# Performance work log

Measured on AMD Instinct MI355X. Metric: run time of the kernel, lower is better.

## Reference

```python
import jax, jax.numpy as jnp
import numpy as np

B, S, D = 4, 4096, 2048
NUM_MODALITIES = 2


def setup_inputs() -> dict:
    key = jax.random.key(0)
    k_x, k_t, k_w0, k_b0, k_w1, k_b1 = jax.random.split(key, 6)
    scale = 1.0 / np.sqrt(D)
    return {
        "hidden_states": jax.random.normal(k_x, (B, S, D), dtype=jnp.float32),
        "type_ids": jax.random.randint(k_t, (B, S), 0, NUM_MODALITIES, dtype=jnp.int32),
        "W0": jax.random.uniform(k_w0, (D, D), jnp.float32, -scale, scale),
        "b0": jax.random.uniform(k_b0, (D,), jnp.float32, -scale, scale),
        "W1": jax.random.uniform(k_w1, (D, D), jnp.float32, -scale, scale),
        "b1": jax.random.uniform(k_b1, (D,), jnp.float32, -scale, scale),
    }


def reference(hidden_states, type_ids, W0, b0, W1, b1):
    # Original: gather tokens where type_ids == i, apply expert i's Linear,
    # scatter into a zero-init [B, S, out_dim] buffer. The masks partition
    # all tokens, so this equals a masked mixture of the two dense GEMMs.
    y0 = jnp.einsum("bsd,ed->bse", hidden_states, W0) + b0  # expert 0
    y1 = jnp.einsum("bsd,ed->bse", hidden_states, W1) + b1  # expert 1
    m0 = (type_ids == 0)[..., None]
    m1 = (type_ids == 1)[..., None]
    zero = jnp.zeros((), dtype=y0.dtype)
    return jnp.where(m0, y0, zero) + jnp.where(m1, y1, zero)
```

## Files before the change

### kernel.cpp

```cpp
#include <hip/hip_runtime.h>
#include <hip/hip_bf16.h>
#include <stdint.h>


#define T_TOK 16384
#define DDIM  2048
#define NT_K  32
#define NT_D  64
#define MT    64
#define NTILE 8

typedef __attribute__((ext_vector_type(4))) float          f32x4;
typedef __attribute__((ext_vector_type(8))) short          bf16x8;
typedef __attribute__((ext_vector_type(2))) unsigned int   u32x2;

#define WS_HBF   0ull
#define WS_W0BF  67108864ull
#define WS_W1BF  75497472ull
#define WS_META  83886080ull
#define WS_IDX   83886208ull
#define WS_NEED  (WS_IDX + 65536ull)

__device__ __forceinline__ unsigned short cvt1_bf16(float f) {
  unsigned u = __builtin_bit_cast(unsigned, f);
  unsigned rnd = 0x7fffu + ((u >> 16) & 1u);
  return (unsigned short)((u + rnd) >> 16);
}

__device__ __forceinline__ void gload_lds16(const void* g, void* l) {
  __builtin_amdgcn_global_load_lds(
      (const __attribute__((address_space(1))) unsigned int*)g,
      (__attribute__((address_space(3))) unsigned int*)l, 16, 0, 0);
}

#define BAR()     asm volatile("s_barrier" ::: "memory")
#define VMCNT2()  asm volatile("s_waitcnt vmcnt(2)" ::: "memory")
#define VMCNT4()  asm volatile("s_waitcnt vmcnt(4)" ::: "memory")
#define VMCNT6()  asm volatile("s_waitcnt vmcnt(6)" ::: "memory")
#define VMCNT0()  asm volatile("s_waitcnt vmcnt(0)" ::: "memory")
#define LGKM0()   asm volatile("s_waitcnt lgkmcnt(0)" ::: "memory")
#define SCHEDBAR() __builtin_amdgcn_sched_barrier(0)

__global__ void k_prep(const float* __restrict__ H, const float* __restrict__ W0,
                       const float* __restrict__ W1, const int* __restrict__ typ,
                       unsigned short* __restrict__ Hbf,
                       unsigned short* __restrict__ W0bf,
                       unsigned short* __restrict__ W1bf,
                       int* __restrict__ meta, int* __restrict__ idx) {
  const int gid = blockIdx.x * blockDim.x + threadIdx.x;
  if (gid < T_TOK) {
    int t = typ[gid];
    int pos = (t == 0) ? atomicAdd(&meta[0], 1)
                       : (T_TOK - 1) - atomicAdd(&meta[1], 1);
    idx[pos] = gid;
  }
  const int nH = T_TOK * DDIM / 4;
  const int nW = DDIM * DDIM / 4;
  const int total = nH + 2 * nW;
  const int stride = gridDim.x * blockDim.x;
  for (int i = gid; i < total; i += stride) {
    const float* s; unsigned short* d; int j;
    if (i < nH)           { s = H;  d = Hbf;  j = i; }
    else if (i < nH + nW) { s = W0; d = W0bf; j = i - nH; }
    else                  { s = W1; d = W1bf; j = i - nH - nW; }
    f32x4 v = ((const f32x4*)s)[j];
    unsigned p0 = (unsigned)cvt1_bf16(v[0]) | ((unsigned)cvt1_bf16(v[1]) << 16);
    unsigned p1 = (unsigned)cvt1_bf16(v[2]) | ((unsigned)cvt1_bf16(v[3]) << 16);
    u32x2 o; o[0] = p0; o[1] = p1;
    ((u32x2*)d)[j] = o;
  }
}

__global__ __launch_bounds__(512) void k_gemm256(
    const unsigned short* __restrict__ Hbf,
    const unsigned short* __restrict__ W0bf,
    const unsigned short* __restrict__ W1bf,
    const float* __restrict__ B0, const float* __restrict__ B1,
    const int* __restrict__ meta, const int* __restrict__ idx,
    float* __restrict__ OUT)
{
  __shared__ char lds[147456];

  const int orig = blockIdx.x;
  const int wg = (orig & 7) * 64 + (orig >> 3);
  int my = wg >> 3;
  const int bx = wg & 7;

  const int c0 = meta[0];
  int ms = c0 >> 8; if (ms > MT - 1) ms = MT - 1;
  my = (my == 0) ? ms : (my == ms) ? 0 : my;

  const int tid  = threadIdx.x;
  const int lane = tid & 63;
  const int wid  = tid >> 6;
  const int wr   = wid >> 2;
  const int wc   = wid & 3;
  const int fr   = lane & 15;
  const int g    = lane >> 4;

  const int start = my * 256;
  const int isDual = (start < c0 && c0 < start + 256) ? 1 : 0;
  const int e0    = (start >= c0) ? 1 : 0;
  const int colBase = bx * 256;

  const int cs = (lane & 3) ^ ((lane >> 3) & 3);
  const char* aS[2];
  int rt[2];
#pragma unroll
  for (int l = 0; l < 2; ++l) {
    int ch = 2 * wid + l;
    rt[l] = ch * 16 + (lane >> 2);
    int orow = idx[start + rt[l]];
    aS[l] = (const char*)Hbf + (size_t)orow * 4096 + cs * 16;
  }
  const int chB = (2 * wid) * 1024;

  const int sw = (g ^ ((fr >> 1) & 3)) << 4;
  int aF[8], bF[4];
#pragma unroll
  for (int m = 0; m < 8; ++m) aF[m] = ((wr * 128 + m * 16 + fr) << 6) + sw;
#pragma unroll
  for (int n = 0; n < 4; ++n) bF[n] = ((wc * 64 + n * 16 + fr) << 6) + sw;

  f32x4 acc[8][4];
#pragma unroll
  for (int m = 0; m < 8; ++m)
#pragma unroll
    for (int n = 0; n < 4; ++n) acc[m][n] = (f32x4)0.0f;

  int cols[4];
#pragma unroll
  for (int n = 0; n < 4; ++n) cols[n] = colBase + wc * 64 + n * 16 + fr;

  if (!isDual) {
    const unsigned short* Wb = e0 ? W1bf : W0bf;
    const char* wS[2];
#pragma unroll
    for (int l = 0; l < 2; ++l)
      wS[l] = (const char*)(Wb + (size_t)(colBase + rt[l]) * DDIM) + cs * 16;

    auto STAGE_A = [&](int d, int kh, int tn) {
      char* dst = lds + (d << 15) + (kh << 14) + chB;
      int ko = tn * 128 + kh * 64;
      gload_lds16(aS[0] + ko, dst);
      gload_lds16(aS[1] + ko, dst + 1024);
    };
    auto STAGE_B = [&](int d, int kh, int tn) {
      char* dst = lds + 65536 + (d << 15) + (kh << 14) + chB;
      int ko = tn * 128 + kh * 64;
      gload_lds16(wS[0] + ko, dst);
      gload_lds16(wS[1] + ko, dst + 1024);
    };

    STAGE_A(0, 0, 0); STAGE_B(0, 0, 0); STAGE_A(0, 1, 0); STAGE_B(0, 1, 0);
    VMCNT4();
    BAR();

#pragma unroll 2
    for (int t = 0; t < NT_K; ++t) {
      const int c = t & 1, d = c ^ 1;
      int t1 = t + 1; if (t1 == NT_K) t1 = NT_K - 1;
      const char* Ak0 = lds + (c << 15);
      const char* Ak1 = Ak0 + 16384;
      const char* Bk0 = lds + 65536 + (c << 15);
      const char* Bk1 = Bk0 + 16384;

      bf16x8 a[8], bb0, bb1;

#pragma unroll
      for (int m = 0; m < 8; ++m) a[m] = *(const bf16x8*)(Ak0 + aF[m]);
      bb0 = *(const bf16x8*)(Bk0 + bF[0]);
      bb1 = *(const bf16x8*)(Bk0 + bF[1]);
      STAGE_A(d, 0, t1);
      BAR(); LGKM0(); SCHEDBAR();
      __builtin_amdgcn_s_setprio(1);
#pragma unroll
      for (int m = 0; m < 8; ++m) {
        acc[m][0] = __builtin_amdgcn_mfma_f32_16x16x32_bf16(a[m], bb0, acc[m][0], 0, 0, 0);
        acc[m][1] = __builtin_amdgcn_mfma_f32_16x16x32_bf16(a[m], bb1, acc[m][1], 0, 0, 0);
      }
      __builtin_amdgcn_s_setprio(0);

      bb0 = *(const bf16x8*)(Bk0 + bF[2]);
      bb1 = *(const bf16x8*)(Bk0 + bF[3]);
      VMCNT2();
      STAGE_B(d, 0, t1);
      BAR(); LGKM0(); SCHEDBAR();
      __builtin_amdgcn_s_setprio(1);
#pragma unroll
      for (int m = 0; m < 8; ++m) {
        acc[m][2] = __builtin_amdgcn_mfma_f32_16x16x32_bf16(a[m], bb0, acc[m][2], 0, 0, 0);
        acc[m][3] = __builtin_amdgcn_mfma_f32_16x16x32_bf16(a[m], bb1, acc[m][3], 0, 0, 0);
      }
      __builtin_amdgcn_s_setprio(0);

#pragma unroll
      for (int m = 0; m < 8; ++m) a[m] = *(const bf16x8*)(Ak1 + aF[m]);
      bb0 = *(const bf16x8*)(Bk1 + bF[0]);
      bb1 = *(const bf16x8*)(Bk1 + bF[1]);
      STAGE_A(d, 1, t1);
      BAR(); LGKM0(); SCHEDBAR();
      __builtin_amdgcn_s_setprio(1);
#pragma unroll
      for (int m = 0; m < 8; ++m) {
        acc[m][0] = __builtin_amdgcn_mfma_f32_16x16x32_bf16(a[m], bb0, acc[m][0], 0, 0, 0);
        acc[m][1] = __builtin_amdgcn_mfma_f32_16x16x32_bf16(a[m], bb1, acc[m][1], 0, 0, 0);
      }
      __builtin_amdgcn_s_setprio(0);

      bb0 = *(const bf16x8*)(Bk1 + bF[2]);
      bb1 = *(const bf16x8*)(Bk1 + bF[3]);
      VMCNT2();
      STAGE_B(d, 1, t1);
      BAR(); LGKM0(); SCHEDBAR();
      __builtin_amdgcn_s_setprio(1);
#pragma unroll
      for (int m = 0; m < 8; ++m) {
        acc[m][2] = __builtin_amdgcn_mfma_f32_16x16x32_bf16(a[m], bb0, acc[m][2], 0, 0, 0);
        acc[m][3] = __builtin_amdgcn_mfma_f32_16x16x32_bf16(a[m], bb1, acc[m][3], 0, 0, 0);
      }
      __builtin_amdgcn_s_setprio(0);
    }

    VMCNT0();

    const float* Bv = e0 ? B1 : B0;
    float bias[4];
#pragma unroll
    for (int n = 0; n < 4; ++n) bias[n] = Bv[cols[n]];
#pragma unroll
    for (int m = 0; m < 8; ++m) {
      int lb = wr * 128 + m * 16 + (g << 2);
#pragma unroll
      for (int j = 0; j < 4; ++j) {
        int orow = idx[start + lb + j];
        float* op = OUT + (size_t)orow * DDIM;
#pragma unroll
        for (int n = 0; n < 4; ++n) op[cols[n]] = acc[m][n][j] + bias[n];
      }
    }
  } else {
    const char* wS0[2]; const char* wS1[2];
#pragma unroll
    for (int l = 0; l < 2; ++l) {
      wS0[l] = (const char*)(W0bf + (size_t)(colBase + rt[l]) * DDIM) + cs * 16;
      wS1[l] = (const char*)(W1bf + (size_t)(colBase + rt[l]) * DDIM) + cs * 16;
    }
    const int lo_w = c0 - start - wr * 128;
    int mmix = 8;
    if (lo_w > 0 && lo_w < 128 && (lo_w & 15)) mmix = lo_w >> 4;

    f32x4 accX[4];
#pragma unroll
    for (int n = 0; n < 4; ++n) accX[n] = (f32x4)0.0f;

    auto DSTAGE = [&](int d, int tn) {
      int ko = tn * 64;
      char* ad  = lds + d * 16384 + chB;
      char* b0d = lds + 49152 + d * 16384 + chB;
      char* b1d = lds + 98304 + d * 16384 + chB;
      gload_lds16(aS[0] + ko, ad);
      gload_lds16(aS[1] + ko, ad + 1024);
      gload_lds16(wS0[0] + ko, b0d);
      gload_lds16(wS0[1] + ko, b0d + 1024);
      gload_lds16(wS1[0] + ko, b1d);
      gload_lds16(wS1[1] + ko, b1d + 1024);
    };

    DSTAGE(0, 0); DSTAGE(1, 1);
    VMCNT6();
    BAR();

    for (int t = 0; t < NT_D; ++t) {
      const int c = t % 3;
      const int d = (t + 2) % 3;
      int t2 = t + 2; if (t2 >= NT_D) t2 = NT_D - 1;
      const char* Ac  = lds + c * 16384;
      const char* B0c = lds + 49152 + c * 16384;
      const char* B1c = lds + 98304 + c * 16384;
      bf16x8 a[8], b0f[4], b1f[4];
#pragma unroll
      for (int m = 0; m < 8; ++m) a[m] = *(const bf16x8*)(Ac + aF[m]);
#pragma unroll
      for (int n = 0; n < 4; ++n) {
        b0f[n] = *(const bf16x8*)(B0c + bF[n]);
        b1f[n] = *(const bf16x8*)(B1c + bF[n]);
      }
      DSTAGE(d, t2);
      VMCNT6();
      BAR(); LGKM0(); SCHEDBAR();
      __builtin_amdgcn_s_setprio(1);
#pragma unroll
      for (int m = 0; m < 8; ++m) {
        if (m == mmix) {
#pragma unroll
          for (int n = 0; n < 4; ++n) {
            acc[m][n] = __builtin_amdgcn_mfma_f32_16x16x32_bf16(a[m], b0f[n], acc[m][n], 0, 0, 0);
            accX[n]   = __builtin_amdgcn_mfma_f32_16x16x32_bf16(a[m], b1f[n], accX[n],   0, 0, 0);
          }
        } else if (m * 16 >= lo_w) {
#pragma unroll
          for (int n = 0; n < 4; ++n)
            acc[m][n] = __builtin_amdgcn_mfma_f32_16x16x32_bf16(a[m], b1f[n], acc[m][n], 0, 0, 0);
        } else {
#pragma unroll
          for (int n = 0; n < 4; ++n)
            acc[m][n] = __builtin_amdgcn_mfma_f32_16x16x32_bf16(a[m], b0f[n], acc[m][n], 0, 0, 0);
        }
      }
      __builtin_amdgcn_s_setprio(0);
      BAR();
    }
    VMCNT0();

    float bias0v[4], bias1v[4];
#pragma unroll
    for (int n = 0; n < 4; ++n) { bias0v[n] = B0[cols[n]]; bias1v[n] = B1[cols[n]]; }
#pragma unroll
    for (int m = 0; m < 8; ++m) {
      int lb = wr * 128 + m * 16 + (g << 2);
      if (m == mmix) {
#pragma unroll
        for (int j = 0; j < 4; ++j) {
          int p = start + lb + j;
          int orow = idx[p];
          float* op = OUT + (size_t)orow * DDIM;
          if (p >= c0) {
#pragma unroll
            for (int n = 0; n < 4; ++n) op[cols[n]] = accX[n][j] + bias1v[n];
          } else {
#pragma unroll
            for (int n = 0; n < 4; ++n) op[cols[n]] = acc[m][n][j] + bias0v[n];
          }
        }
      } else {
        int em = (m * 16 >= lo_w) ? 1 : 0;
#pragma unroll
        for (int j = 0; j < 4; ++j) {
          int orow = idx[start + lb + j];
          float* op = OUT + (size_t)orow * DDIM;
#pragma unroll
          for (int n = 0; n < 4; ++n)
            op[cols[n]] = acc[m][n][j] + (em ? bias1v[n] : bias0v[n]);
        }
      }
    }
  }
}

#define BMd 64
#define BNd 64
#define BKd 32
#define LDW 36

__device__ __forceinline__ bf16x8 cvt_bf16x8(f32x4 lo, f32x4 hi) {
  bf16x8 r;
#pragma unroll
  for (int i = 0; i < 4; ++i) {
    r[i]     = (short)cvt1_bf16(lo[i]);
    r[i + 4] = (short)cvt1_bf16(hi[i]);
  }
  return r;
}

__global__ __launch_bounds__(256, 2) void mot_mfma_diag(
    const float* __restrict__ H,  const int* __restrict__ TYP,
    const float* __restrict__ W0, const float* __restrict__ B0,
    const float* __restrict__ W1, const float* __restrict__ B1,
    float* __restrict__ OUT)
{
  __shared__ float As[BMd * LDW];
  __shared__ float W0s[BNd * LDW];
  __shared__ float W1s[BNd * LDW];

  const int tid = threadIdx.x;
  const int rowBase = blockIdx.y * BMd;
  const int colBase = blockIdx.x * BNd;
  const int srow  = tid >> 3;
  const int scol4 = (tid & 7) << 2;
  const float* hA  = H  + (size_t)(rowBase + srow) * DDIM + scol4;
  const float* hW0 = W0 + (size_t)(colBase + srow) * DDIM + scol4;
  const float* hW1 = W1 + (size_t)(colBase + srow) * DDIM + scol4;

  const int lane = tid & 63;
  const int w    = tid >> 6;
  const int fr   = lane & 15;
  const int g    = lane >> 4;

  f32x4 acc0[4], acc1[4];
#pragma unroll
  for (int m = 0; m < 4; ++m) { acc0[m] = (f32x4)0.0f; acc1[m] = (f32x4)0.0f; }

  for (int k0 = 0; k0 < DDIM; k0 += BKd) {
    f32x4 va[2], v0[2], v1[2];
#pragma unroll
    for (int p = 0; p < 2; ++p) {
      va[p] = *(const f32x4*)(hA  + (size_t)p * 32 * DDIM);
      v0[p] = *(const f32x4*)(hW0 + (size_t)p * 32 * DDIM);
      v1[p] = *(const f32x4*)(hW1 + (size_t)p * 32 * DDIM);
    }
    hA += BKd; hW0 += BKd; hW1 += BKd;
    __syncthreads();
#pragma unroll
    for (int p = 0; p < 2; ++p) {
      int r = srow + 32 * p;
      *(f32x4*)(&As [r * LDW + scol4]) = va[p];
      *(f32x4*)(&W0s[r * LDW + scol4]) = v0[p];
      *(f32x4*)(&W1s[r * LDW + scol4]) = v1[p];
    }
    __syncthreads();

    bf16x8 af[4];
#pragma unroll
    for (int m = 0; m < 4; ++m) {
      const float* ap = &As[(m * 16 + fr) * LDW + g * 8];
      af[m] = cvt_bf16x8(*(const f32x4*)ap, *(const f32x4*)(ap + 4));
    }
    const float* b0p = &W0s[(w * 16 + fr) * LDW + g * 8];
    const float* b1p = &W1s[(w * 16 + fr) * LDW + g * 8];
    bf16x8 bf0 = cvt_bf16x8(*(const f32x4*)b0p, *(const f32x4*)(b0p + 4));
    bf16x8 bf1 = cvt_bf16x8(*(const f32x4*)b1p, *(const f32x4*)(b1p + 4));
#pragma unroll
    for (int m = 0; m < 4; ++m) {
      acc0[m] = __builtin_amdgcn_mfma_f32_16x16x32_bf16(af[m], bf0, acc0[m], 0, 0, 0);
      acc1[m] = __builtin_amdgcn_mfma_f32_16x16x32_bf16(af[m], bf1, acc1[m], 0, 0, 0);
    }
  }

  const int col = colBase + w * 16 + fr;
  const float bz0 = B0[col];
  const float bz1 = B1[col];
#pragma unroll
  for (int m = 0; m < 4; ++m)
#pragma unroll
    for (int j = 0; j < 4; ++j) {
      int row = rowBase + m * 16 + (g << 2) + j;
      int t = TYP[row];
      OUT[(size_t)row * DDIM + col] = (t == 0) ? (acc0[m][j] + bz0) : (acc1[m][j] + bz1);
    }
}

extern "C" void kernel_launch(void* const* d_in, const int* in_sizes, int n_in,
                              void* d_out, int out_size, void* d_ws, size_t ws_size,
                              hipStream_t stream) {
  const float* H   = (const float*)d_in[0];
  const int*   TYP = (const int*)  d_in[1];
  const float* W0  = (const float*)d_in[2];
  const float* B0v = (const float*)d_in[3];
  const float* W1  = (const float*)d_in[4];
  const float* B1v = (const float*)d_in[5];
  float* OUT = (float*)d_out;

  if (ws_size < WS_NEED) {
    dim3 grid(DDIM / BNd, T_TOK / BMd);
    mot_mfma_diag<<<grid, dim3(256), 0, stream>>>(H, TYP, W0, B0v, W1, B1v, OUT);
    return;
  }

  unsigned short* Hbf  = (unsigned short*)((char*)d_ws + WS_HBF);
  unsigned short* W0bf = (unsigned short*)((char*)d_ws + WS_W0BF);
  unsigned short* W1bf = (unsigned short*)((char*)d_ws + WS_W1BF);
  int* meta = (int*)((char*)d_ws + WS_META);
  int* idx  = (int*)((char*)d_ws + WS_IDX);

  hipMemsetAsync(meta, 0, 16, stream);
  k_prep<<<4096, 256, 0, stream>>>(H, W0, W1, TYP, Hbf, W0bf, W1bf, meta, idx);
  k_gemm256<<<MT * NTILE, 512, 0, stream>>>(Hbf, W0bf, W1bf, B0v, B1v, meta, idx, OUT);
}
```

Baseline: 215.9 us.

## Split mixed-expert tile into smaller blocks to shorten the dual-GEMM straggler

The single row tile where both experts mix is no longer computed by 8 large blocks doing two GEMMs. It is handled by 32 separate 256x64 blocks, each splitting its warps across W0 and W1 loads, while the 504 single-expert blocks keep the original 256x256 path. The goal is to stop the dual-GEMM tiles, which cost twice as much, from being the tail of the launch. In exchange the dual blocks use smaller tiles with lower operand reuse, a shallower double-buffered pipeline, and a slightly larger grid.

```diff
diff --git a/kernel.cpp b/kernel.cpp
--- a/kernel.cpp
+++ b/kernel.cpp
@@ -8,7 +8,6 @@
 #define NT_K  32
 #define NT_D  64
 #define MT    64
-#define NTILE 8
 
 typedef __attribute__((ext_vector_type(4))) float          f32x4;
 typedef __attribute__((ext_vector_type(8))) short          bf16x8;
@@ -35,8 +34,8 @@
 
 #define BAR()     asm volatile("s_barrier" ::: "memory")
 #define VMCNT2()  asm volatile("s_waitcnt vmcnt(2)" ::: "memory")
+#define VMCNT3()  asm volatile("s_waitcnt vmcnt(3)" ::: "memory")
 #define VMCNT4()  asm volatile("s_waitcnt vmcnt(4)" ::: "memory")
-#define VMCNT6()  asm volatile("s_waitcnt vmcnt(6)" ::: "memory")
 #define VMCNT0()  asm volatile("s_waitcnt vmcnt(0)" ::: "memory")
 #define LGKM0()   asm volatile("s_waitcnt lgkmcnt(0)" ::: "memory")
 #define SCHEDBAR() __builtin_amdgcn_sched_barrier(0)
@@ -79,60 +78,55 @@
     const int* __restrict__ meta, const int* __restrict__ idx,
     float* __restrict__ OUT)
 {
-  __shared__ char lds[147456];
-
-  const int orig = blockIdx.x;
-  const int wg = (orig & 7) * 64 + (orig >> 3);
-  int my = wg >> 3;
-  const int bx = wg & 7;
+  __shared__ char lds[131072];
 
   const int c0 = meta[0];
   int ms = c0 >> 8; if (ms > MT - 1) ms = MT - 1;
-  my = (my == 0) ? ms : (my == ms) ? 0 : my;
 
   const int tid  = threadIdx.x;
   const int lane = tid & 63;
   const int wid  = tid >> 6;
-  const int wr   = wid >> 2;
-  const int wc   = wid & 3;
   const int fr   = lane & 15;
   const int g    = lane >> 4;
-
-  const int start = my * 256;
-  const int isDual = (start < c0 && c0 < start + 256) ? 1 : 0;
-  const int e0    = (start >= c0) ? 1 : 0;
-  const int colBase = bx * 256;
-
-  const int cs = (lane & 3) ^ ((lane >> 3) & 3);
-  const char* aS[2];
-  int rt[2];
-#pragma unroll
-  for (int l = 0; l < 2; ++l) {
-    int ch = 2 * wid + l;
-    rt[l] = ch * 16 + (lane >> 2);
-    int orow = idx[start + rt[l]];
-    aS[l] = (const char*)Hbf + (size_t)orow * 4096 + cs * 16;
-  }
-  const int chB = (2 * wid) * 1024;
-
-  const int sw = (g ^ ((fr >> 1) & 3)) << 4;
-  int aF[8], bF[4];
-#pragma unroll
-  for (int m = 0; m < 8; ++m) aF[m] = ((wr * 128 + m * 16 + fr) << 6) + sw;
-#pragma unroll
-  for (int n = 0; n < 4; ++n) bF[n] = ((wc * 64 + n * 16 + fr) << 6) + sw;
-
-  f32x4 acc[8][4];
-#pragma unroll
-  for (int m = 0; m < 8; ++m)
-#pragma unroll
-    for (int n = 0; n < 4; ++n) acc[m][n] = (f32x4)0.0f;
-
-  int cols[4];
-#pragma unroll
-  for (int n = 0; n < 4; ++n) cols[n] = colBase + wc * 64 + n * 16 + fr;
-
-  if (!isDual) {
+  const int cs   = (lane & 3) ^ ((lane >> 3) & 3);
+  const int sw   = (g ^ ((fr >> 1) & 3)) << 4;
+
+  if (blockIdx.x < 504) {
+    const int orig = blockIdx.x;
+    const int wg = (orig & 7) * 63 + (orig >> 3);
+    int i_t = wg >> 3;
+    const int bx = wg & 7;
+    const int my = i_t + (i_t >= ms ? 1 : 0);
+
+    const int wr = wid >> 2;
+    const int wc = wid & 3;
+    const int start = my * 256;
+    const int e0 = (start >= c0) ? 1 : 0;
+    const int colBase = bx * 256;
+
+    const char* aS[2];
+    int rt[2];
+#pragma unroll
+    for (int l = 0; l < 2; ++l) {
+      int ch = 2 * wid + l;
+      rt[l] = ch * 16 + (lane >> 2);
+      int orow = idx[start + rt[l]];
+      aS[l] = (const char*)Hbf + (size_t)orow * 4096 + cs * 16;
+    }
+    const int chB = (2 * wid) * 1024;
+
+    int aF[8], bF[4];
+#pragma unroll
+    for (int m = 0; m < 8; ++m) aF[m] = ((wr * 128 + m * 16 + fr) << 6) + sw;
+#pragma unroll
+    for (int n = 0; n < 4; ++n) bF[n] = ((wc * 64 + n * 16 + fr) << 6) + sw;
+
+    f32x4 acc[8][4];
+#pragma unroll
+    for (int m = 0; m < 8; ++m)
+#pragma unroll
+      for (int n = 0; n < 4; ++n) acc[m][n] = (f32x4)0.0f;
+
     const unsigned short* Wb = e0 ? W1bf : W0bf;
     const char* wS[2];
 #pragma unroll
@@ -226,8 +220,12 @@
 
     const float* Bv = e0 ? B1 : B0;
     float bias[4];
-#pragma unroll
-    for (int n = 0; n < 4; ++n) bias[n] = Bv[cols[n]];
+    int cols[4];
+#pragma unroll
+    for (int n = 0; n < 4; ++n) {
+      cols[n] = colBase + wc * 64 + n * 16 + fr;
+      bias[n] = Bv[cols[n]];
+    }
 #pragma unroll
     for (int m = 0; m < 8; ++m) {
       int lb = wr * 128 + m * 16 + (g << 2);
@@ -240,71 +238,88 @@
       }
     }
   } else {
-    const char* wS0[2]; const char* wS1[2];
+    const int sub = blockIdx.x - 504;
+    const int bx = sub >> 2;
+    const int nq = sub & 3;
+    const int colBase = bx * 256 + nq * 64;
+    const int start = ms * 256;
+
+    const int wr = wid >> 1;
+    const int wc = wid & 1;
+
+    const char* aS[2];
 #pragma unroll
     for (int l = 0; l < 2; ++l) {
-      wS0[l] = (const char*)(W0bf + (size_t)(colBase + rt[l]) * DDIM) + cs * 16;
-      wS1[l] = (const char*)(W1bf + (size_t)(colBase + rt[l]) * DDIM) + cs * 16;
-    }
-    const int lo_w = c0 - start - wr * 128;
+      int r_t = (2 * wid + l) * 16 + (lane >> 2);
+      int orow = idx[start + r_t];
+      aS[l] = (const char*)Hbf + (size_t)orow * 4096 + cs * 16;
+    }
+    const unsigned short* Wbs = (wid < 4) ? W0bf : W1bf;
+    const int bchunk = wid & 3;
+    const char* bS = (const char*)(Wbs + (size_t)(colBase + bchunk * 16 + (lane >> 2)) * DDIM) + cs * 16;
+
+    int aF[4], bF[2];
+#pragma unroll
+    for (int m = 0; m < 4; ++m) aF[m] = ((wr * 64 + m * 16 + fr) << 6) + sw;
+#pragma unroll
+    for (int n = 0; n < 2; ++n) bF[n] = ((wc * 32 + n * 16 + fr) << 6) + sw;
+
+    const int lo_w = c0 - start - wr * 64;
     int mmix = 8;
-    if (lo_w > 0 && lo_w < 128 && (lo_w & 15)) mmix = lo_w >> 4;
-
-    f32x4 accX[4];
-#pragma unroll
-    for (int n = 0; n < 4; ++n) accX[n] = (f32x4)0.0f;
+    if (lo_w > 0 && lo_w < 64 && (lo_w & 15)) mmix = lo_w >> 4;
+
+    f32x4 acc[4][2], accX[2];
+#pragma unroll
+    for (int m = 0; m < 4; ++m) { acc[m][0] = (f32x4)0.0f; acc[m][1] = (f32x4)0.0f; }
+    accX[0] = (f32x4)0.0f; accX[1] = (f32x4)0.0f;
 
     auto DSTAGE = [&](int d, int tn) {
       int ko = tn * 64;
-      char* ad  = lds + d * 16384 + chB;
-      char* b0d = lds + 49152 + d * 16384 + chB;
-      char* b1d = lds + 98304 + d * 16384 + chB;
-      gload_lds16(aS[0] + ko, ad);
-      gload_lds16(aS[1] + ko, ad + 1024);
-      gload_lds16(wS0[0] + ko, b0d);
-      gload_lds16(wS0[1] + ko, b0d + 1024);
-      gload_lds16(wS1[0] + ko, b1d);
-      gload_lds16(wS1[1] + ko, b1d + 1024);
+      char* ad = lds + d * 24576;
+      gload_lds16(aS[0] + ko, ad + (2 * wid) * 1024);
+      gload_lds16(aS[1] + ko, ad + (2 * wid + 1) * 1024);
+      char* bd = ad + 16384 + (wid < 4 ? 0 : 4096) + bchunk * 1024;
+      gload_lds16(bS + ko, bd);
     };
 
-    DSTAGE(0, 0); DSTAGE(1, 1);
-    VMCNT6();
+    DSTAGE(0, 0);
+    VMCNT0();
     BAR();
 
     for (int t = 0; t < NT_D; ++t) {
-      const int c = t % 3;
-      const int d = (t + 2) % 3;
-      int t2 = t + 2; if (t2 >= NT_D) t2 = NT_D - 1;
-      const char* Ac  = lds + c * 16384;
-      const char* B0c = lds + 49152 + c * 16384;
-      const char* B1c = lds + 98304 + c * 16384;
-      bf16x8 a[8], b0f[4], b1f[4];
-#pragma unroll
-      for (int m = 0; m < 8; ++m) a[m] = *(const bf16x8*)(Ac + aF[m]);
-#pragma unroll
-      for (int n = 0; n < 4; ++n) {
+      const int c = t & 1, d = c ^ 1;
+      int t1 = t + 1; if (t1 == NT_D) t1 = NT_D - 1;
+      DSTAGE(d, t1);
+      VMCNT3();
+      BAR();
+      const char* Ac  = lds + c * 24576;
+      const char* B0c = Ac + 16384;
+      const char* B1c = Ac + 20480;
+      bf16x8 a[4], b0f[2], b1f[2];
+#pragma unroll
+      for (int m = 0; m < 4; ++m) a[m] = *(const bf16x8*)(Ac + aF[m]);
+#pragma unroll
+      for (int n = 0; n < 2; ++n) {
         b0f[n] = *(const bf16x8*)(B0c + bF[n]);
         b1f[n] = *(const bf16x8*)(B1c + bF[n]);
       }
-      DSTAGE(d, t2);
-      VMCNT6();
-      BAR(); LGKM0(); SCHEDBAR();
+      LGKM0(); SCHEDBAR();
       __builtin_amdgcn_s_setprio(1);
 #pragma unroll
-      for (int m = 0; m < 8; ++m) {
+      for (int m = 0; m < 4; ++m) {
         if (m == mmix) {
 #pragma unroll
-          for (int n = 0; n < 4; ++n) {
+          for (int n = 0; n < 2; ++n) {
             acc[m][n] = __builtin_amdgcn_mfma_f32_16x16x32_bf16(a[m], b0f[n], acc[m][n], 0, 0, 0);
             accX[n]   = __builtin_amdgcn_mfma_f32_16x16x32_bf16(a[m], b1f[n], accX[n],   0, 0, 0);
           }
         } else if (m * 16 >= lo_w) {
 #pragma unroll
-          for (int n = 0; n < 4; ++n)
+          for (int n = 0; n < 2; ++n)
             acc[m][n] = __builtin_amdgcn_mfma_f32_16x16x32_bf16(a[m], b1f[n], acc[m][n], 0, 0, 0);
         } else {
 #pragma unroll
-          for (int n = 0; n < 4; ++n)
+          for (int n = 0; n < 2; ++n)
             acc[m][n] = __builtin_amdgcn_mfma_f32_16x16x32_bf16(a[m], b0f[n], acc[m][n], 0, 0, 0);
         }
       }
@@ -313,35 +328,29 @@
     }
     VMCNT0();
 
-    float bias0v[4], bias1v[4];
-#pragma unroll
-    for (int n = 0; n < 4; ++n) { bias0v[n] = B0[cols[n]]; bias1v[n] = B1[cols[n]]; }
-#pragma unroll
-    for (int m = 0; m < 8; ++m) {
-      int lb = wr * 128 + m * 16 + (g << 2);
-      if (m == mmix) {
-#pragma unroll
-        for (int j = 0; j < 4; ++j) {
-          int p = start + lb + j;
-          int orow = idx[p];
-          float* op = OUT + (size_t)orow * DDIM;
-          if (p >= c0) {
-#pragma unroll
-            for (int n = 0; n < 4; ++n) op[cols[n]] = accX[n][j] + bias1v[n];
-          } else {
-#pragma unroll
-            for (int n = 0; n < 4; ++n) op[cols[n]] = acc[m][n][j] + bias0v[n];
-          }
-        }
-      } else {
-        int em = (m * 16 >= lo_w) ? 1 : 0;
-#pragma unroll
-        for (int j = 0; j < 4; ++j) {
-          int orow = idx[start + lb + j];
-          float* op = OUT + (size_t)orow * DDIM;
-#pragma unroll
-          for (int n = 0; n < 4; ++n)
-            op[cols[n]] = acc[m][n][j] + (em ? bias1v[n] : bias0v[n]);
+    int cols[2];
+    float bias0v[2], bias1v[2];
+#pragma unroll
+    for (int n = 0; n < 2; ++n) {
+      cols[n] = colBase + wc * 32 + n * 16 + fr;
+      bias0v[n] = B0[cols[n]];
+      bias1v[n] = B1[cols[n]];
+    }
+#pragma unroll
+    for (int m = 0; m < 4; ++m) {
+#pragma unroll
+      for (int j = 0; j < 4; ++j) {
+        int p = start + wr * 64 + m * 16 + (g << 2) + j;
+        int orow = idx[p];
+        float* op = OUT + (size_t)orow * DDIM;
+        int e1r = (p >= c0) ? 1 : 0;
+        if (m == mmix && e1r) {
+#pragma unroll
+          for (int n = 0; n < 2; ++n) op[cols[n]] = accX[n][j] + bias1v[n];
+        } else {
+#pragma unroll
+          for (int n = 0; n < 2; ++n)
+            op[cols[n]] = acc[m][n][j] + (e1r ? bias1v[n] : bias0v[n]);
         }
       }
     }
@@ -465,5 +474,5 @@
 
   hipMemsetAsync(meta, 0, 16, stream);
   k_prep<<<4096, 256, 0, stream>>>(H, W0, W1, TYP, Hbf, W0bf, W1bf, meta, idx);
-  k_gemm256<<<MT * NTILE, 512, 0, stream>>>(Hbf, W0bf, W1bf, B0v, B1v, meta, idx, OUT);
-}
+  k_gemm256<<<536, 512, 0, stream>>>(Hbf, W0bf, W1bf, B0v, B1v, meta, idx, OUT);
+}
```

Result: faster. 210.5 us (-2.5%).
